# Optimization experiments

Hardware: AMD Instinct MI355X
Metric: run time of the kernel (lower is better)

The kernel has to match this reference:

```python
import jax, jax.numpy as jnp
import numpy as np


def setup_inputs() -> dict:
    key = jax.random.key(0)
    ks = jax.random.split(key, 7)
    B, D, d1, d2, d3 = 256, 256, 1024, 512, 256
    s = lambda f: 1.0 / np.sqrt(f)  # torch nn.Linear-style init scale
    return {
        "x": jax.random.normal(ks[0], (B, D), jnp.float32),
        "W1": jax.random.normal(ks[1], (d1, D), jnp.float32) * s(D),
        "b1": jax.random.normal(ks[2], (d1,), jnp.float32) * s(D),
        "W2": jax.random.normal(ks[3], (d2, d1), jnp.float32) * s(d1),
        "b2": jax.random.normal(ks[4], (d2,), jnp.float32) * s(d1),
        "W3": jax.random.normal(ks[5], (d3, d2), jnp.float32) * s(d2),
        "b3": jax.random.normal(ks[6], (d3,), jnp.float32) * s(d2),
        "k": 10,
    }


def _border_dists(x, W1, b1, W2, b2, W3, b3):
    # Layer 1: pre-activations and boundary distances. For the first layer the
    # effective linear map is W1 itself (shared across the batch).
    z1 = x @ W1.T + b1                                   # [B, d1]
    dist1 = jnp.abs(z1) / jnp.linalg.norm(W1, axis=1)    # [B, d1]
    m1 = (z1 > 0).astype(x.dtype)
    V1 = m1[:, :, None] * W1[None]                       # [B, d1, D] per-instance map after ReLU
    h1 = m1 * z1

    # Layer 2
    z2 = h1 @ W2.T + b2                                  # [B, d2]
    V2 = jnp.einsum('oi,bid->bod', W2, V1)               # [B, d2, D]
    dist2 = jnp.abs(z2) / jnp.linalg.norm(V2, axis=2)
    m2 = (z2 > 0).astype(x.dtype)
    h2 = m2 * z2

    # Layer 3
    z3 = h2 @ W3.T + b3                                  # [B, d3]
    V3 = jnp.einsum('oi,bid->bod', W3, m2[:, :, None] * V2)  # [B, d3, D]
    dist3 = jnp.abs(z3) / jnp.linalg.norm(V3, axis=2)

    return jnp.concatenate([dist1, dist2, dist3], axis=1)  # [B, d1+d2+d3]


def reference(x, W1, b1, W2, b2, W3, b3, k):
    dists = _border_dists(x, W1, b1, W2, b2, W3, b3)
    # smallest-k distances per instance via top_k on negated distances
    neg_top, _ = jax.lax.top_k(-dists, k)                # [B, k]
    return jnp.sum(-neg_top)                             # border-distance loss (scalar)
```

## Files before the change

### kernel.cpp

```cpp
#include <hip/hip_runtime.h>
#include <math.h>
#include <float.h>

#define B   256
#define D   256
#define D1  1024
#define D2  512
#define D3  256
#define NDIST (D1 + D2 + D3)
#define CQ  2.0f

typedef __attribute__((ext_vector_type(8))) short short8;
typedef __attribute__((ext_vector_type(4))) float f32x4;
typedef __attribute__((ext_vector_type(4))) int   i32x4;

__device__ __forceinline__ float waveReduceSum(float v) {
    #pragma unroll
    for (int off = 32; off > 0; off >>= 1)
        v += __shfl_down(v, off, 64);
    return v;
}
__device__ __forceinline__ float waveReduceMax(float v) {
    #pragma unroll
    for (int off = 32; off > 0; off >>= 1)
        v = fmaxf(v, __shfl_down(v, off, 64));
    return v;
}
__device__ __forceinline__ unsigned short f2bf(float f) {
    unsigned int u = __float_as_uint(f);
    u = (u + 0x7FFFu + ((u >> 16) & 1u)) >> 16;
    return (unsigned short)u;
}
__device__ __forceinline__ float bf2f(unsigned short h) {
    return __uint_as_float(((unsigned int)h) << 16);
}
__device__ __forceinline__ void gld16(const void* g, void* l) {
    __builtin_amdgcn_global_load_lds(
        (const __attribute__((address_space(1))) unsigned int*)g,
        (__attribute__((address_space(3))) unsigned int*)l, 16, 0, 0);
}
__device__ __forceinline__ int swz_src(int row, int lane) {
    return ((lane & 3) + ((row >> 1) & 3)) & 3;
}
__device__ __forceinline__ int swz_frag(int row, int quad) {
    return row * 32 + (((quad - ((row >> 1) & 3)) & 3) * 8);
}

__global__ __launch_bounds__(256) void k_prep(
    const float* __restrict__ x,  const float* __restrict__ W1,
    const float* __restrict__ W2, const float* __restrict__ W3,
    float* __restrict__ zeros,
    float* __restrict__ outp,
    unsigned short* __restrict__ xhi,  unsigned short* __restrict__ xlo,
    unsigned short* __restrict__ W1hi, unsigned short* __restrict__ W1lo,
    unsigned short* __restrict__ W2hi, unsigned short* __restrict__ W2lo,
    unsigned short* __restrict__ W3hi, unsigned short* __restrict__ W3lo,
    signed char* __restrict__ W1Ti8, float* __restrict__ saq,
    signed char* __restrict__ W2i8,  float* __restrict__ sbq,
    signed char* __restrict__ W3i8,  float* __restrict__ s3q,
    float* __restrict__ rn1) {
    int blk = blockIdx.x;
    int t = threadIdx.x;
    if (blk < 1536) {
        if (blk == 0 && t == 0) outp[0] = 0.f;
        zeros[blk * 256 + t] = 0.f;
        return;
    }
    if (blk < 2496) {
        int i4 = ((blk - 1536) * 256 + t) * 4;
        const float* src; unsigned short *hi, *lo; int off;
        if (i4 < 65536)       { src = x;  hi = xhi;  lo = xlo;  off = i4; }
        else if (i4 < 327680) { src = W1; hi = W1hi; lo = W1lo; off = i4 - 65536; }
        else if (i4 < 851968) { src = W2; hi = W2hi; lo = W2lo; off = i4 - 327680; }
        else                  { src = W3; hi = W3hi; lo = W3lo; off = i4 - 851968; }
        float4 v = *(const float4*)(src + off);
        ushort4 h, l;
        h.x = f2bf(v.x); l.x = f2bf(v.x - bf2f(h.x));
        h.y = f2bf(v.y); l.y = f2bf(v.y - bf2f(h.y));
        h.z = f2bf(v.z); l.z = f2bf(v.z - bf2f(h.z));
        h.w = f2bf(v.w); l.w = f2bf(v.w - bf2f(h.w));
        *(ushort4*)(hi + off) = h;
        *(ushort4*)(lo + off) = l;
        return;
    }
    if (blk < 2528) {
        int ty = t >> 5, tx = t & 31;
        int d = (blk - 2496) * 8 + ty;
        float m = 0.f;
        for (int i = tx; i < D1; i += 32) m = fmaxf(m, fabsf(W1[(size_t)i * D + d]));
        #pragma unroll
        for (int off = 16; off > 0; off >>= 1) m = fmaxf(m, __shfl_down(m, off, 32));
        m = __shfl(m, 0, 32);
        m = fmaxf(m, 1e-20f);
        if (tx == 0) saq[d] = m / 127.f;
        float inv = 127.f / m;
        for (int i = tx; i < D1; i += 32) {
            int q = __float2int_rn(W1[(size_t)i * D + d] * inv);
            W1Ti8[(size_t)d * D1 + i] = (signed char)q;
        }
        return;
    }
    if (blk < 2656) {
        int o = (blk - 2528) * 4 + (t >> 6);
        int l = t & 63;
        const float* row = W2 + (size_t)o * D1;
        float m = 0.f;
        for (int tt = l; tt < D1; tt += 64) m = fmaxf(m, fabsf(row[tt]));
        m = waveReduceMax(m);
        m = __shfl(m, 0, 64);
        m = fmaxf(m, 1e-20f);
        if (l == 0) sbq[o] = m / 127.f;
        float inv = 127.f / m;
        for (int tt = l; tt < D1; tt += 64)
            W2i8[(size_t)o * D1 + tt] = (signed char)__float2int_rn(row[tt] * inv);
        return;
    }
    if (blk < 2720) {
        int p = (blk - 2656) * 4 + (t >> 6);
        int l = t & 63;
        const float* row = W3 + (size_t)p * D2;
        float m = 0.f;
        for (int tt = l; tt < D2; tt += 64) m = fmaxf(m, fabsf(row[tt]));
        m = waveReduceMax(m);
        m = __shfl(m, 0, 64);
        m = fmaxf(m, 1e-20f);
        if (l == 0) s3q[p] = m / 127.f;
        float inv = 127.f / m;
        for (int tt = l; tt < D2; tt += 64)
            W3i8[(size_t)p * D2 + tt] = (signed char)__float2int_rn(row[tt] * inv);
        return;
    }
    {
        int gw = (blk - 2720) * 4 + (t >> 6);
        int lane = t & 63;
        const float* row = W1 + (size_t)gw * D;
        float s = 0.f;
        for (int tt = lane; tt < D; tt += 64) { float v = row[tt]; s += v * v; }
        s = waveReduceSum(s);
        if (lane == 0) rn1[gw] = sqrtf(s);
    }
}

template <int KD, int KL>
__device__ __forceinline__ void mfma3_64(
    const unsigned short* __restrict__ Ahi, const unsigned short* __restrict__ Alo,
    const unsigned short* __restrict__ Bhi, const unsigned short* __restrict__ Blo,
    int m0, int n0, int k0, unsigned short* sm, f32x4 acc[2][2]) {
    int tid = threadIdx.x;
    int l = tid & 63, w = tid >> 6;
    int rsub = l >> 2;
    int quad = l >> 4, l16 = l & 15;
    int wm = (w >> 1) * 32, wn = (w & 1) * 32;
    unsigned short* sAh = sm;
    unsigned short* sAl = sm + 2048;
    unsigned short* sBh = sm + 4096;
    unsigned short* sBl = sm + 6144;
    ptrdiff_t dA = Alo - Ahi, dB = Blo - Bhi;
    int rloc = w * 16 + rsub;
    int c = swz_src(rloc, l);
    const unsigned short* pa = Ahi + (size_t)(m0 + rloc) * KD + k0 + c * 8;
    const unsigned short* pb = Bhi + (size_t)(n0 + rloc) * KD + k0 + c * 8;
    int aoff[2], boff[2];
    #pragma unroll
    for (int mt = 0; mt < 2; mt++) aoff[mt] = swz_frag(wm + mt * 16 + l16, quad);
    #pragma unroll
    for (int nt = 0; nt < 2; nt++) boff[nt] = swz_frag(wn + nt * 16 + l16, quad);
    for (int kk = 0; kk < KL; kk += 32) {
        gld16(pa + kk,      sAh + w * 512);
        gld16(pa + dA + kk, sAl + w * 512);
        gld16(pb + kk,      sBh + w * 512);
        gld16(pb + dB + kk, sBl + w * 512);
        __syncthreads();
        short8 ah[2], al[2], bh[2], bl[2];
        #pragma unroll
        for (int mt = 0; mt < 2; mt++) {
            ah[mt] = *(const short8*)(sAh + aoff[mt]);
            al[mt] = *(const short8*)(sAl + aoff[mt]);
        }
        #pragma unroll
        for (int nt = 0; nt < 2; nt++) {
            bh[nt] = *(const short8*)(sBh + boff[nt]);
            bl[nt] = *(const short8*)(sBl + boff[nt]);
        }
        #pragma unroll
        for (int mt = 0; mt < 2; mt++)
            #pragma unroll
            for (int nt = 0; nt < 2; nt++) {
                acc[mt][nt] = __builtin_amdgcn_mfma_f32_16x16x32_bf16(ah[mt], bh[nt], acc[mt][nt], 0, 0, 0);
                acc[mt][nt] = __builtin_amdgcn_mfma_f32_16x16x32_bf16(ah[mt], bl[nt], acc[mt][nt], 0, 0, 0);
                acc[mt][nt] = __builtin_amdgcn_mfma_f32_16x16x32_bf16(al[mt], bh[nt], acc[mt][nt], 0, 0, 0);
            }
        __syncthreads();
    }
}

__global__ __launch_bounds__(256) void k_l1(
    const unsigned short* __restrict__ xhi,  const unsigned short* __restrict__ xlo,
    const unsigned short* __restrict__ W1hi, const unsigned short* __restrict__ W1lo,
    const float* __restrict__ b1, const float* __restrict__ rn1,
    float* __restrict__ dists, unsigned char* __restrict__ m1q,
    unsigned short* __restrict__ h1hi, unsigned short* __restrict__ h1lo) {
    __shared__ __align__(16) unsigned short sm[8192];
    int m0 = blockIdx.x * 64, n0 = blockIdx.y * 64;
    f32x4 acc[2][2] = {};
    mfma3_64<D, D>(xhi, xlo, W1hi, W1lo, m0, n0, 0, sm, acc);
    int l = threadIdx.x & 63, w = threadIdx.x >> 6;
    int quad = l >> 4, l16 = l & 15;
    int wm = (w >> 1) * 32, wn = (w & 1) * 32;
    #pragma unroll
    for (int mt = 0; mt < 2; mt++)
        #pragma unroll
        for (int nt = 0; nt < 2; nt++) {
            int n = n0 + wn + nt * 16 + l16;
            float bv = b1[n], rv = rn1[n];
            #pragma unroll
            for (int r = 0; r < 4; r++) {
                int m = m0 + wm + mt * 16 + quad * 4 + r;
                float z = acc[mt][nt][r] + bv;
                size_t idx = (size_t)m * D1 + n;
                dists[idx] = fabsf(z) / rv;
                m1q[idx] = (z > 0.f) ? 0xFFu : 0u;
                float h = z > 0.f ? z : 0.f;
                unsigned short hh = f2bf(h);
                h1hi[idx] = hh;
                h1lo[idx] = f2bf(h - bf2f(hh));
            }
        }
}

__global__ __launch_bounds__(256) void k_big1(
    const unsigned short* __restrict__ h1hi, const unsigned short* __restrict__ h1lo,
    const unsigned short* __restrict__ W2hi, const unsigned short* __restrict__ W2lo,
    float* __restrict__ z2,
    const signed char* __restrict__ W1Ti8,
    const signed char* __restrict__ W2i8,
    const unsigned char* __restrict__ m1q,
    const float* __restrict__ saq,
    const float* __restrict__ sbq,
    signed char* __restrict__ qV2,
    float* __restrict__ norm2) {
    __shared__ __align__(16) unsigned char smem[32768];
    int bid = blockIdx.x;

    if (bid < 128) {
        unsigned short* sm = (unsigned short*)smem;
        int m0 = (bid & 3) * 64, n0 = ((bid >> 2) & 7) * 64, k0 = (bid >> 5) * 256;
        f32x4 acc[2][2] = {};
        mfma3_64<D1, 256>(h1hi, h1lo, W2hi, W2lo, m0, n0, k0, sm, acc);
        int l = threadIdx.x & 63, w = threadIdx.x >> 6;
        int quad = l >> 4, l16 = l & 15;
        int wm = (w >> 1) * 32, wn = (w & 1) * 32;
        #pragma unroll
        for (int mt = 0; mt < 2; mt++)
            #pragma unroll
            for (int nt = 0; nt < 2; nt++) {
                int n = n0 + wn + nt * 16 + l16;
                #pragma unroll
                for (int r = 0; r < 4; r++) {
                    int m = m0 + wm + mt * 16 + quad * 4 + r;
                    atomicAdd(&z2[(size_t)m * D2 + n], acc[mt][nt][r]);
                }
            }
        return;
    }

    int j = bid - 128;
    signed char* As = (signed char*)smem;
    signed char* Bs = (signed char*)smem + 16384;
    int m0 = (j & 1) * 128;
    int o0 = ((j >> 1) & 3) * 128;
    int b = j >> 3;
    int tid = threadIdx.x;
    int l = tid & 63, w = tid >> 6;
    int quad = l >> 4, l16 = l & 15;
    int wm = (w >> 1) * 64, wn = (w & 1) * 64;
    const unsigned char* mrow = m1q + (size_t)b * D1;

    const signed char* pa[4];
    const signed char* pb[4];
    int lrow = l >> 3, ls = l & 7;
    #pragma unroll
    for (int r = 0; r < 4; r++) {
        int row = r * 32 + w * 8 + lrow;
        int c = (ls + (row & 7)) & 7;
        pa[r] = W1Ti8 + (size_t)(m0 + row) * D1 + c * 16;
        pb[r] = W2i8 + (size_t)(o0 + row) * D1 + c * 16;
    }
    int aoff[4][2], boff[4][2];
    #pragma unroll
    for (int mt = 0; mt < 4; mt++) {
        int tr = wm + mt * 16 + l16;
        #pragma unroll
        for (int ks = 0; ks < 2; ks++)
            aoff[mt][ks] = tr * 128 + (((ks * 4 + quad) - (tr & 7)) & 7) * 16;
    }
    #pragma unroll
    for (int nt = 0; nt < 4; nt++) {
        int tr = wn + nt * 16 + l16;
        #pragma unroll
        for (int ks = 0; ks < 2; ks++)
            boff[nt][ks] = tr * 128 + (((ks * 4 + quad) - (tr & 7)) & 7) * 16;
    }

    i32x4 acc[4][4];
    #pragma unroll
    for (int i = 0; i < 4; i++)
        #pragma unroll
        for (int jj = 0; jj < 4; jj++) acc[i][jj] = (i32x4)0;

    for (int kk = 0; kk < D1; kk += 128) {
        #pragma unroll
        for (int r = 0; r < 4; r++) {
            gld16(pa[r] + kk, As + r * 4096 + w * 1024);
            gld16(pb[r] + kk, Bs + r * 4096 + w * 1024);
        }
        i32x4 mv0 = *(const i32x4*)(mrow + kk + quad * 16);
        i32x4 mv1 = *(const i32x4*)(mrow + kk + 64 + quad * 16);
        __syncthreads();
        #pragma unroll
        for (int ks = 0; ks < 2; ks++) {
            i32x4 mv = ks ? mv1 : mv0;
            i32x4 a[4], bq[4];
            #pragma unroll
            for (int mt = 0; mt < 4; mt++)
                a[mt] = (*(const i32x4*)(As + aoff[mt][ks])) & mv;
            #pragma unroll
            for (int nt = 0; nt < 4; nt++)
                bq[nt] = *(const i32x4*)(Bs + boff[nt][ks]);
            #pragma unroll
            for (int mt = 0; mt < 4; mt++)
                #pragma unroll
                for (int nt = 0; nt < 4; nt++)
                    acc[mt][nt] = __builtin_amdgcn_mfma_i32_16x16x64_i8(
                        a[mt], bq[nt], acc[mt][nt], 0, 0, 0);
        }
        __syncthreads();
    }

    float sad[4][4];
    #pragma unroll
    for (int mt = 0; mt < 4; mt++)
        #pragma unroll
        for (int r = 0; r < 4; r++)
            sad[mt][r] = saq[m0 + wm + mt * 16 + quad * 4 + r];
    float sbv[4], sbdq[4];
    #pragma unroll
    for (int nt = 0; nt < 4; nt++) {
        sbv[nt] = sbq[o0 + wn + nt * 16 + l16];
        sbdq[nt] = sbv[nt] * (1.0f / CQ);
    }

    #pragma unroll
    for (int nt = 0; nt < 4; nt++) {
        float s = 0.f;
        #pragma unroll
        for (int mt = 0; mt < 4; mt++)
            #pragma unroll
            for (int r = 0; r < 4; r++) {
                float v = (float)acc[mt][nt][r] * sad[mt][r] * sbv[nt];
                s += v * v;
            }
        s += __shfl_down(s, 32, 64);
        s += __shfl_down(s, 16, 64);
        if (l < 16)
            atomicAdd(&norm2[(size_t)b * D2 + o0 + wn + nt * 16 + l], s);
    }

    signed char* qb = qV2 + (size_t)b * (D * D2);
    #pragma unroll
    for (int mt = 0; mt < 4; mt++) {
        int dbase = m0 + wm + mt * 16 + quad * 4;
        #pragma unroll
        for (int r = 0; r < 4; r++)
            #pragma unroll
            for (int nt = 0; nt < 4; nt++) {
                int o = o0 + wn + nt * 16 + l16;
                int qi = __float2int_rn((float)acc[mt][nt][r] * sbdq[nt]);
                qi = max(-127, min(127, qi));
                qb[(size_t)(dbase + r) * D2 + o] = (signed char)qi;
            }
    }
}

__global__ __launch_bounds__(256) void k_big2(
    const float* __restrict__ z2,
    const float* __restrict__ b2,
    const unsigned short* __restrict__ W3hi, const unsigned short* __restrict__ W3lo,
    float* __restrict__ z3,
    const signed char* __restrict__ W3i8,
    const signed char* __restrict__ qV2,
    const float* __restrict__ saq,
    const float* __restrict__ s3q,
    float* __restrict__ norm3) {
    __shared__ __align__(16) unsigned char smem[33280];
    int bid = blockIdx.x;
    int tid = threadIdx.x;

    if (bid < 32) {
        unsigned short* sAh = (unsigned short*)smem;
        unsigned short* sAl = sAh + 2048;
        unsigned short* sBh = sAh + 4096;
        unsigned short* sBl = sAh + 6144;
        int m0 = (bid & 3) * 64, n0 = ((bid >> 2) & 3) * 64, k0 = (bid >> 4) * 256;
        int l = tid & 63, w = tid >> 6;
        int rsub = l >> 2;
        int quad = l >> 4, l16 = l & 15;
        int wm = (w >> 1) * 32, wn = (w & 1) * 32;
        int rloc = w * 16 + rsub;
        int c = swz_src(rloc, l);
        const float* pz  = z2 + (size_t)(m0 + rloc) * D2 + k0 + c * 8;
        const float* pbi = b2 + k0 + c * 8;
        const unsigned short* pb = W3hi + (size_t)(n0 + rloc) * D2 + k0 + c * 8;
        ptrdiff_t dB = W3lo - W3hi;
        int aoff[2], boff[2];
        #pragma unroll
        for (int mt = 0; mt < 2; mt++) aoff[mt] = swz_frag(wm + mt * 16 + l16, quad);
        #pragma unroll
        for (int nt = 0; nt < 2; nt++) boff[nt] = swz_frag(wn + nt * 16 + l16, quad);
        int wrA = w * 512 + l * 8;
        f32x4 acc[2][2] = {};
        for (int kk = 0; kk < 256; kk += 32) {
            gld16(pb + kk,      sBh + w * 512);
            gld16(pb + dB + kk, sBl + w * 512);
            float4 za = *(const float4*)(pz + kk);
            float4 zb = *(const float4*)(pz + kk + 4);
            float4 ba = *(const float4*)(pbi + kk);
            float4 bb = *(const float4*)(pbi + kk + 4);
            float hv[8] = { za.x + ba.x, za.y + ba.y, za.z + ba.z, za.w + ba.w,
                            zb.x + bb.x, zb.y + bb.y, zb.z + bb.z, zb.w + bb.w };
            short8 h8, l8;
            #pragma unroll
            for (int q2 = 0; q2 < 8; q2++) {
                float h = hv[q2] > 0.f ? hv[q2] : 0.f;
                unsigned short hh = f2bf(h);
                h8[q2] = (short)hh;
                l8[q2] = (short)f2bf(h - bf2f(hh));
            }
            *(short8*)(sAh + wrA) = h8;
            *(short8*)(sAl + wrA) = l8;
            __syncthreads();
            short8 ah[2], al[2], bh[2], bl[2];
            #pragma unroll
            for (int mt = 0; mt < 2; mt++) {
                ah[mt] = *(const short8*)(sAh + aoff[mt]);
                al[mt] = *(const short8*)(sAl + aoff[mt]);
            }
            #pragma unroll
            for (int nt = 0; nt < 2; nt++) {
                bh[nt] = *(const short8*)(sBh + boff[nt]);
                bl[nt] = *(const short8*)(sBl + boff[nt]);
            }
            #pragma unroll
            for (int mt = 0; mt < 2; mt++)
                #pragma unroll
                for (int nt = 0; nt < 2; nt++) {
                    acc[mt][nt] = __builtin_amdgcn_mfma_f32_16x16x32_bf16(ah[mt], bh[nt], acc[mt][nt], 0, 0, 0);
                    acc[mt][nt] = __builtin_amdgcn_mfma_f32_16x16x32_bf16(ah[mt], bl[nt], acc[mt][nt], 0, 0, 0);
                    acc[mt][nt] = __builtin_amdgcn_mfma_f32_16x16x32_bf16(al[mt], bh[nt], acc[mt][nt], 0, 0, 0);
                }
            __syncthreads();
        }
        #pragma unroll
        for (int mt = 0; mt < 2; mt++)
            #pragma unroll
            for (int nt = 0; nt < 2; nt++) {
                int n = n0 + wn + nt * 16 + l16;
                #pragma unroll
                for (int r = 0; r < 4; r++) {
                    int m = m0 + wm + mt * 16 + quad * 4 + r;
                    atomicAdd(&z3[(size_t)m * D3 + n], acc[mt][nt][r]);
                }
            }
        return;
    }

    int j = bid - 32;
    signed char* As = (signed char*)smem;
    signed char* Bs = (signed char*)smem + 16384;
    unsigned char* mbuf = (unsigned char*)smem + 32768;
    int m0 = (j & 1) * 128;
    int n0 = ((j >> 1) & 1) * 128;
    int bc = j >> 2;
    int l = tid & 63, w = tid >> 6;
    int quad = l >> 4, l16 = l & 15;
    int wm = (w >> 1) * 64, wn = (w & 1) * 64;
    const signed char* Bsrc = qV2 + (size_t)bc * (D * D2);

    {
        #pragma unroll
        for (int rr = 0; rr < 2; rr++) {
            int o = tid * 2 + rr;
            float z = z2[(size_t)bc * D2 + o] + b2[o];
            mbuf[o] = (z > 0.f) ? 0xFFu : 0u;
        }
    }
    __syncthreads();

    const signed char* pa[4];
    const signed char* pb[4];
    int lrow = l >> 3, ls = l & 7;
    #pragma unroll
    for (int r = 0; r < 4; r++) {
        int row = r * 32 + w * 8 + lrow;
        int c = (ls + (row & 7)) & 7;
        pa[r] = W3i8 + (size_t)(m0 + row) * D2 + c * 16;
        pb[r] = Bsrc + (size_t)(n0 + row) * D2 + c * 16;
    }
    int aoff[4][2], boff[4][2];
    #pragma unroll
    for (int mt = 0; mt < 4; mt++) {
        int tr = wm + mt * 16 + l16;
        #pragma unroll
        for (int ks = 0; ks < 2; ks++)
            aoff[mt][ks] = tr * 128 + (((ks * 4 + quad) - (tr & 7)) & 7) * 16;
    }
    #pragma unroll
    for (int nt = 0; nt < 4; nt++) {
        int tr = wn + nt * 16 + l16;
        #pragma unroll
        for (int ks = 0; ks < 2; ks++)
            boff[nt][ks] = tr * 128 + (((ks * 4 + quad) - (tr & 7)) & 7) * 16;
    }

    i32x4 acc[4][4];
    #pragma unroll
    for (int i = 0; i < 4; i++)
        #pragma unroll
        for (int jj = 0; jj < 4; jj++) acc[i][jj] = (i32x4)0;

    for (int kk = 0; kk < D2; kk += 128) {
        #pragma unroll
        for (int r = 0; r < 4; r++) {
            gld16(pa[r] + kk, As + r * 4096 + w * 1024);
            gld16(pb[r] + kk, Bs + r * 4096 + w * 1024);
        }
        __syncthreads();
        i32x4 mv0 = *(const i32x4*)(mbuf + kk + quad * 16);
        i32x4 mv1 = *(const i32x4*)(mbuf + kk + 64 + quad * 16);
        #pragma unroll
        for (int ks = 0; ks < 2; ks++) {
            i32x4 mv = ks ? mv1 : mv0;
            i32x4 a[4], bq[4];
            #pragma unroll
            for (int mt = 0; mt < 4; mt++)
                a[mt] = *(const i32x4*)(As + aoff[mt][ks]);
            #pragma unroll
            for (int nt = 0; nt < 4; nt++)
                bq[nt] = (*(const i32x4*)(Bs + boff[nt][ks])) & mv;
            #pragma unroll
            for (int mt = 0; mt < 4; mt++)
                #pragma unroll
                for (int nt = 0; nt < 4; nt++)
                    acc[mt][nt] = __builtin_amdgcn_mfma_i32_16x16x64_i8(
                        a[mt], bq[nt], acc[mt][nt], 0, 0, 0);
        }
        __syncthreads();
    }

    float saCQ[4];
    #pragma unroll
    for (int nt = 0; nt < 4; nt++)
        saCQ[nt] = saq[n0 + wn + nt * 16 + l16] * CQ;

    #pragma unroll
    for (int mt = 0; mt < 4; mt++)
        #pragma unroll
        for (int r = 0; r < 4; r++) {
            float s = 0.f;
            #pragma unroll
            for (int nt = 0; nt < 4; nt++) {
                float v = (float)acc[mt][nt][r] * saCQ[nt];
                s += v * v;
            }
            s += __shfl_down(s, 8, 64);
            s += __shfl_down(s, 4, 64);
            s += __shfl_down(s, 2, 64);
            s += __shfl_down(s, 1, 64);
            if (l16 == 0) {
                int p = m0 + wm + mt * 16 + quad * 4 + r;
                float s3 = s3q[p];
                atomicAdd(&norm3[(size_t)bc * D3 + p], s * s3 * s3);
            }
        }
}

__global__ __launch_bounds__(256) void k_topk(
    const float* __restrict__ dists,
    const float* __restrict__ z2, const float* __restrict__ b2,
    const float* __restrict__ norm2,
    const float* __restrict__ z3, const float* __restrict__ b3,
    const float* __restrict__ norm3,
    const int* __restrict__ kp, float* __restrict__ outp) {
    int t = threadIdx.x;
    int wv = t >> 6, lane = t & 63;
    int b = blockIdx.x * 4 + wv;
    float lv[28];
    #pragma unroll
    for (int j = 0; j < 16; j++)
        lv[j] = dists[(size_t)b * D1 + lane + 64 * j];
    #pragma unroll
    for (int j = 16; j < 24; j++) {
        int o = lane + 64 * (j - 16);
        float zz = z2[(size_t)b * D2 + o] + b2[o];
        lv[j] = fabsf(zz) / sqrtf(norm2[(size_t)b * D2 + o]);
    }
    #pragma unroll
    for (int j = 24; j < 28; j++) {
        int p = lane + 64 * (j - 24);
        float zz = z3[(size_t)b * D3 + p] + b3[p];
        lv[j] = fabsf(zz) / sqrtf(norm3[(size_t)b * D3 + p]);
    }
    int k = *kp;
    if (k > NDIST) k = NDIST;
    float sum = 0.f;
    for (int it = 0; it < k; it++) {
        float mv = lv[0]; int mj = 0;
        #pragma unroll
        for (int j = 1; j < 28; j++)
            if (lv[j] < mv) { mv = lv[j]; mj = j; }
        unsigned long long key =
            ((unsigned long long)__float_as_uint(mv) << 32) | (unsigned)(lane * 32 + mj);
        #pragma unroll
        for (int off = 1; off < 64; off <<= 1) {
            unsigned long long o = __shfl_xor(key, off, 64);
            if (o < key) key = o;
        }
        sum += __uint_as_float((unsigned)(key >> 32));
        int wl = (int)((key >> 5) & 63u), wj = (int)(key & 31u);
        if (lane == wl) lv[wj] = FLT_MAX;
    }
    if (lane == 0) atomicAdd(outp, sum);
}

extern "C" void kernel_launch(void* const* d_in, const int* in_sizes, int n_in,
                              void* d_out, int out_size, void* d_ws, size_t ws_size,
                              hipStream_t stream) {
    const float* x  = (const float*)d_in[0];
    const float* W1 = (const float*)d_in[1];
    const float* b1 = (const float*)d_in[2];
    const float* W2 = (const float*)d_in[3];
    const float* b2 = (const float*)d_in[4];
    const float* W3 = (const float*)d_in[5];
    const float* b3 = (const float*)d_in[6];
    const int*   kp = (const int*)d_in[7];
    float* outp = (float*)d_out;

    float* fp = (float*)d_ws;
    float* rn1     = fp;                          fp += D1;
    float* dists   = fp;                          fp += (size_t)B * D1;
    float* saq     = fp;                          fp += D;
    float* sbq     = fp;                          fp += D2;
    float* s3q     = fp;                          fp += D3;
    float* z2      = fp;                          fp += (size_t)B * D2;
    float* z3      = fp;                          fp += (size_t)B * D3;
    float* norm2   = fp;                          fp += (size_t)B * D2;
    float* norm3   = fp;                          fp += (size_t)B * D3;
    unsigned short* up = (unsigned short*)fp;
    unsigned short* W2hi  = up;  up += (size_t)D2 * D1;
    unsigned short* W2lo  = up;  up += (size_t)D2 * D1;
    unsigned short* W3hi  = up;  up += (size_t)D3 * D2;
    unsigned short* W3lo  = up;  up += (size_t)D3 * D2;
    unsigned short* xhi   = up;  up += (size_t)B * D;
    unsigned short* xlo   = up;  up += (size_t)B * D;
    unsigned short* W1hi  = up;  up += (size_t)D1 * D;
    unsigned short* W1lo  = up;  up += (size_t)D1 * D;
    unsigned short* h1hi  = up;  up += (size_t)B * D1;
    unsigned short* h1lo  = up;  up += (size_t)B * D1;
    signed char*    cp = (signed char*)up;
    signed char*    W1Ti8 = cp;  cp += (size_t)D * D1;
    signed char*    W2i8  = cp;  cp += (size_t)D2 * D1;
    signed char*    W3i8  = cp;  cp += (size_t)D3 * D2;
    unsigned char*  m1q   = (unsigned char*)cp;  cp += (size_t)B * D1;
    signed char*    qV2   = cp;

    k_prep<<<2976, 256, 0, stream>>>(x, W1, W2, W3, z2, outp,
                                     xhi, xlo, W1hi, W1lo, W2hi, W2lo, W3hi, W3lo,
                                     W1Ti8, saq, W2i8, sbq, W3i8, s3q, rn1);

    k_l1<<<dim3(B / 64, D1 / 64), 256, 0, stream>>>(xhi, xlo, W1hi, W1lo, b1, rn1,
                                                    dists, m1q, h1hi, h1lo);

    k_big1<<<2176, 256, 0, stream>>>(h1hi, h1lo, W2hi, W2lo, z2,
                                     W1Ti8, W2i8, m1q, saq, sbq, qV2, norm2);

    k_big2<<<1056, 256, 0, stream>>>(z2, b2, W3hi, W3lo, z3,
                                     W3i8, qV2, saq, s3q, norm3);

    k_topk<<<B / 4, 256, 0, stream>>>(dists, z2, b2, norm2, z3, b3, norm3, kp, outp);
}
```

Measured before the change: 181.2 us.

## Split prep kernel and co-schedule layer-1 GEMM with remaining weight prep

The monolithic prep kernel is split. A small first kernel now converts only x and W1 to bf16 hi/lo and computes the W1 row norms. The layer-1 GEMM then runs in one launch together with zeroing, the W2/W3 bf16 splits and the int8 quantizations, so the 64 GEMM blocks overlap with independent prep work instead of waiting for all of it. Zeroing also switches to float4 stores with fewer blocks. The GEMM blocks are placed first so they get scheduled early, and the launch count stays the same.

```diff
diff --git a/kernel.cpp b/kernel.cpp
--- a/kernel.cpp
+++ b/kernel.cpp
@@ -46,92 +46,35 @@
     return row * 32 + (((quad - ((row >> 1) & 3)) & 3) * 8);
 }
 
-__global__ __launch_bounds__(256) void k_prep(
-    const float* __restrict__ x,  const float* __restrict__ W1,
-    const float* __restrict__ W2, const float* __restrict__ W3,
-    float* __restrict__ zeros,
-    float* __restrict__ outp,
+__device__ __forceinline__ void split_job(const float* src, unsigned short* hi,
+                                          unsigned short* lo, int off) {
+    float4 v = *(const float4*)(src + off);
+    ushort4 h, l;
+    h.x = f2bf(v.x); l.x = f2bf(v.x - bf2f(h.x));
+    h.y = f2bf(v.y); l.y = f2bf(v.y - bf2f(h.y));
+    h.z = f2bf(v.z); l.z = f2bf(v.z - bf2f(h.z));
+    h.w = f2bf(v.w); l.w = f2bf(v.w - bf2f(h.w));
+    *(ushort4*)(hi + off) = h;
+    *(ushort4*)(lo + off) = l;
+}
+
+__global__ __launch_bounds__(256) void k_prepA(
+    const float* __restrict__ x, const float* __restrict__ W1,
     unsigned short* __restrict__ xhi,  unsigned short* __restrict__ xlo,
     unsigned short* __restrict__ W1hi, unsigned short* __restrict__ W1lo,
-    unsigned short* __restrict__ W2hi, unsigned short* __restrict__ W2lo,
-    unsigned short* __restrict__ W3hi, unsigned short* __restrict__ W3lo,
-    signed char* __restrict__ W1Ti8, float* __restrict__ saq,
-    signed char* __restrict__ W2i8,  float* __restrict__ sbq,
-    signed char* __restrict__ W3i8,  float* __restrict__ s3q,
     float* __restrict__ rn1) {
     int blk = blockIdx.x;
     int t = threadIdx.x;
-    if (blk < 1536) {
-        if (blk == 0 && t == 0) outp[0] = 0.f;
-        zeros[blk * 256 + t] = 0.f;
-        return;
-    }
-    if (blk < 2496) {
-        int i4 = ((blk - 1536) * 256 + t) * 4;
-        const float* src; unsigned short *hi, *lo; int off;
-        if (i4 < 65536)       { src = x;  hi = xhi;  lo = xlo;  off = i4; }
-        else if (i4 < 327680) { src = W1; hi = W1hi; lo = W1lo; off = i4 - 65536; }
-        else if (i4 < 851968) { src = W2; hi = W2hi; lo = W2lo; off = i4 - 327680; }
-        else                  { src = W3; hi = W3hi; lo = W3lo; off = i4 - 851968; }
-        float4 v = *(const float4*)(src + off);
-        ushort4 h, l;
-        h.x = f2bf(v.x); l.x = f2bf(v.x - bf2f(h.x));
-        h.y = f2bf(v.y); l.y = f2bf(v.y - bf2f(h.y));
-        h.z = f2bf(v.z); l.z = f2bf(v.z - bf2f(h.z));
-        h.w = f2bf(v.w); l.w = f2bf(v.w - bf2f(h.w));
-        *(ushort4*)(hi + off) = h;
-        *(ushort4*)(lo + off) = l;
-        return;
-    }
-    if (blk < 2528) {
-        int ty = t >> 5, tx = t & 31;
-        int d = (blk - 2496) * 8 + ty;
-        float m = 0.f;
-        for (int i = tx; i < D1; i += 32) m = fmaxf(m, fabsf(W1[(size_t)i * D + d]));
-        #pragma unroll
-        for (int off = 16; off > 0; off >>= 1) m = fmaxf(m, __shfl_down(m, off, 32));
-        m = __shfl(m, 0, 32);
-        m = fmaxf(m, 1e-20f);
-        if (tx == 0) saq[d] = m / 127.f;
-        float inv = 127.f / m;
-        for (int i = tx; i < D1; i += 32) {
-            int q = __float2int_rn(W1[(size_t)i * D + d] * inv);
-            W1Ti8[(size_t)d * D1 + i] = (signed char)q;
-        }
-        return;
-    }
-    if (blk < 2656) {
-        int o = (blk - 2528) * 4 + (t >> 6);
-        int l = t & 63;
-        const float* row = W2 + (size_t)o * D1;
-        float m = 0.f;
-        for (int tt = l; tt < D1; tt += 64) m = fmaxf(m, fabsf(row[tt]));
-        m = waveReduceMax(m);
-        m = __shfl(m, 0, 64);
-        m = fmaxf(m, 1e-20f);
-        if (l == 0) sbq[o] = m / 127.f;
-        float inv = 127.f / m;
-        for (int tt = l; tt < D1; tt += 64)
-            W2i8[(size_t)o * D1 + tt] = (signed char)__float2int_rn(row[tt] * inv);
-        return;
-    }
-    if (blk < 2720) {
-        int p = (blk - 2656) * 4 + (t >> 6);
-        int l = t & 63;
-        const float* row = W3 + (size_t)p * D2;
-        float m = 0.f;
-        for (int tt = l; tt < D2; tt += 64) m = fmaxf(m, fabsf(row[tt]));
-        m = waveReduceMax(m);
-        m = __shfl(m, 0, 64);
-        m = fmaxf(m, 1e-20f);
-        if (l == 0) s3q[p] = m / 127.f;
-        float inv = 127.f / m;
-        for (int tt = l; tt < D2; tt += 64)
-            W3i8[(size_t)p * D2 + tt] = (signed char)__float2int_rn(row[tt] * inv);
+    if (blk < 64) {
+        split_job(x, xhi, xlo, blk * 1024 + t * 4);
+        return;
+    }
+    if (blk < 320) {
+        split_job(W1, W1hi, W1lo, (blk - 64) * 1024 + t * 4);
         return;
     }
     {
-        int gw = (blk - 2720) * 4 + (t >> 6);
+        int gw = (blk - 320) * 4 + (t >> 6);
         int lane = t & 63;
         const float* row = W1 + (size_t)gw * D;
         float s = 0.f;
@@ -194,38 +137,112 @@
     }
 }
 
-__global__ __launch_bounds__(256) void k_l1(
+__global__ __launch_bounds__(256) void k_l1p(
+    const float* __restrict__ W1, const float* __restrict__ W2,
+    const float* __restrict__ W3,
     const unsigned short* __restrict__ xhi,  const unsigned short* __restrict__ xlo,
     const unsigned short* __restrict__ W1hi, const unsigned short* __restrict__ W1lo,
     const float* __restrict__ b1, const float* __restrict__ rn1,
     float* __restrict__ dists, unsigned char* __restrict__ m1q,
-    unsigned short* __restrict__ h1hi, unsigned short* __restrict__ h1lo) {
+    unsigned short* __restrict__ h1hi, unsigned short* __restrict__ h1lo,
+    float* __restrict__ zeros, float* __restrict__ outp,
+    unsigned short* __restrict__ W2hi, unsigned short* __restrict__ W2lo,
+    unsigned short* __restrict__ W3hi, unsigned short* __restrict__ W3lo,
+    signed char* __restrict__ W1Ti8, float* __restrict__ saq,
+    signed char* __restrict__ W2i8,  float* __restrict__ sbq,
+    signed char* __restrict__ W3i8,  float* __restrict__ s3q) {
     __shared__ __align__(16) unsigned short sm[8192];
-    int m0 = blockIdx.x * 64, n0 = blockIdx.y * 64;
-    f32x4 acc[2][2] = {};
-    mfma3_64<D, D>(xhi, xlo, W1hi, W1lo, m0, n0, 0, sm, acc);
-    int l = threadIdx.x & 63, w = threadIdx.x >> 6;
-    int quad = l >> 4, l16 = l & 15;
-    int wm = (w >> 1) * 32, wn = (w & 1) * 32;
-    #pragma unroll
-    for (int mt = 0; mt < 2; mt++)
-        #pragma unroll
-        for (int nt = 0; nt < 2; nt++) {
-            int n = n0 + wn + nt * 16 + l16;
-            float bv = b1[n], rv = rn1[n];
-            #pragma unroll
-            for (int r = 0; r < 4; r++) {
-                int m = m0 + wm + mt * 16 + quad * 4 + r;
-                float z = acc[mt][nt][r] + bv;
-                size_t idx = (size_t)m * D1 + n;
-                dists[idx] = fabsf(z) / rv;
-                m1q[idx] = (z > 0.f) ? 0xFFu : 0u;
-                float h = z > 0.f ? z : 0.f;
-                unsigned short hh = f2bf(h);
-                h1hi[idx] = hh;
-                h1lo[idx] = f2bf(h - bf2f(hh));
-            }
-        }
+    int blk = blockIdx.x;
+    int t = threadIdx.x;
+
+    if (blk < 64) {
+        int m0 = (blk & 3) * 64, n0 = (blk >> 2) * 64;
+        f32x4 acc[2][2] = {};
+        mfma3_64<D, D>(xhi, xlo, W1hi, W1lo, m0, n0, 0, sm, acc);
+        int l = t & 63, w = t >> 6;
+        int quad = l >> 4, l16 = l & 15;
+        int wm = (w >> 1) * 32, wn = (w & 1) * 32;
+        #pragma unroll
+        for (int mt = 0; mt < 2; mt++)
+            #pragma unroll
+            for (int nt = 0; nt < 2; nt++) {
+                int n = n0 + wn + nt * 16 + l16;
+                float bv = b1[n], rv = rn1[n];
+                #pragma unroll
+                for (int r = 0; r < 4; r++) {
+                    int m = m0 + wm + mt * 16 + quad * 4 + r;
+                    float z = acc[mt][nt][r] + bv;
+                    size_t idx = (size_t)m * D1 + n;
+                    dists[idx] = fabsf(z) / rv;
+                    m1q[idx] = (z > 0.f) ? 0xFFu : 0u;
+                    float h = z > 0.f ? z : 0.f;
+                    unsigned short hh = f2bf(h);
+                    h1hi[idx] = hh;
+                    h1lo[idx] = f2bf(h - bf2f(hh));
+                }
+            }
+        return;
+    }
+    if (blk < 448) {
+        if (blk == 64 && t == 0) outp[0] = 0.f;
+        int i4 = (blk - 64) * 1024 + t * 4;
+        *(float4*)(zeros + i4) = make_float4(0.f, 0.f, 0.f, 0.f);
+        return;
+    }
+    if (blk < 960) {
+        split_job(W2, W2hi, W2lo, (blk - 448) * 1024 + t * 4);
+        return;
+    }
+    if (blk < 1088) {
+        split_job(W3, W3hi, W3lo, (blk - 960) * 1024 + t * 4);
+        return;
+    }
+    if (blk < 1120) {
+        int ty = t >> 5, tx = t & 31;
+        int d = (blk - 1088) * 8 + ty;
+        float m = 0.f;
+        for (int i = tx; i < D1; i += 32) m = fmaxf(m, fabsf(W1[(size_t)i * D + d]));
+        #pragma unroll
+        for (int off = 16; off > 0; off >>= 1) m = fmaxf(m, __shfl_down(m, off, 32));
+        m = __shfl(m, 0, 32);
+        m = fmaxf(m, 1e-20f);
+        if (tx == 0) saq[d] = m / 127.f;
+        float inv = 127.f / m;
+        for (int i = tx; i < D1; i += 32) {
+            int q = __float2int_rn(W1[(size_t)i * D + d] * inv);
+            W1Ti8[(size_t)d * D1 + i] = (signed char)q;
+        }
+        return;
+    }
+    if (blk < 1248) {
+        int o = (blk - 1120) * 4 + (t >> 6);
+        int l = t & 63;
+        const float* row = W2 + (size_t)o * D1;
+        float m = 0.f;
+        for (int tt = l; tt < D1; tt += 64) m = fmaxf(m, fabsf(row[tt]));
+        m = waveReduceMax(m);
+        m = __shfl(m, 0, 64);
+        m = fmaxf(m, 1e-20f);
+        if (l == 0) sbq[o] = m / 127.f;
+        float inv = 127.f / m;
+        for (int tt = l; tt < D1; tt += 64)
+            W2i8[(size_t)o * D1 + tt] = (signed char)__float2int_rn(row[tt] * inv);
+        return;
+    }
+    {
+        int p = (blk - 1248) * 4 + (t >> 6);
+        int l = t & 63;
+        const float* row = W3 + (size_t)p * D2;
+        float m = 0.f;
+        for (int tt = l; tt < D2; tt += 64) m = fmaxf(m, fabsf(row[tt]));
+        m = waveReduceMax(m);
+        m = __shfl(m, 0, 64);
+        m = fmaxf(m, 1e-20f);
+        if (l == 0) s3q[p] = m / 127.f;
+        float inv = 127.f / m;
+        for (int tt = l; tt < D2; tt += 64)
+            W3i8[(size_t)p * D2 + tt] = (signed char)__float2int_rn(row[tt] * inv);
+    }
 }
 
 __global__ __launch_bounds__(256) void k_big1(
@@ -673,12 +690,12 @@
     unsigned char*  m1q   = (unsigned char*)cp;  cp += (size_t)B * D1;
     signed char*    qV2   = cp;
 
-    k_prep<<<2976, 256, 0, stream>>>(x, W1, W2, W3, z2, outp,
-                                     xhi, xlo, W1hi, W1lo, W2hi, W2lo, W3hi, W3lo,
-                                     W1Ti8, saq, W2i8, sbq, W3i8, s3q, rn1);
-
-    k_l1<<<dim3(B / 64, D1 / 64), 256, 0, stream>>>(xhi, xlo, W1hi, W1lo, b1, rn1,
-                                                    dists, m1q, h1hi, h1lo);
+    k_prepA<<<576, 256, 0, stream>>>(x, W1, xhi, xlo, W1hi, W1lo, rn1);
+
+    k_l1p<<<1312, 256, 0, stream>>>(W1, W2, W3, xhi, xlo, W1hi, W1lo, b1, rn1,
+                                    dists, m1q, h1hi, h1lo,
+                                    z2, outp, W2hi, W2lo, W3hi, W3lo,
+                                    W1Ti8, saq, W2i8, sbq, W3i8, s3q);
 
     k_big1<<<2176, 256, 0, stream>>>(h1hi, h1lo, W2hi, W2lo, z2,
                                      W1Ti8, W2i8, m1q, saq, sbq, qV2, norm2);
```

After: 177.9 us. Within noise of the previous version (-1.8%).
